# Kernel tuning notes

Hardware: AMD Instinct MI355X
Metric: run time of the kernel (lower is better)

## Reference

```python
import jax, jax.numpy as jnp
import numpy as np

INPUT_DIM = 16
HIDDEN_DIM = 2048
OUTPUT_DIM = 3
SEQ_LEN = 8192


def setup_inputs() -> dict:
    key = jax.random.key(0)
    ks = jax.random.split(key, 9)
    s = 1.0 / np.sqrt(HIDDEN_DIM)  # PyTorch LSTMCell/Linear init scale
    return {
        "state_action": jax.random.normal(ks[0], (SEQ_LEN, INPUT_DIM), dtype=jnp.float32),
        "W_ih": jax.random.uniform(ks[1], (4 * HIDDEN_DIM, INPUT_DIM), jnp.float32, -s, s),
        "W_hh": jax.random.uniform(ks[2], (4 * HIDDEN_DIM, HIDDEN_DIM), jnp.float32, -s, s),
        "b_ih": jax.random.uniform(ks[3], (4 * HIDDEN_DIM,), jnp.float32, -s, s),
        "b_hh": jax.random.uniform(ks[4], (4 * HIDDEN_DIM,), jnp.float32, -s, s),
        "W_uvw": jax.random.uniform(ks[5], (OUTPUT_DIM, HIDDEN_DIM), jnp.float32, -s, s),
        "b_uvw": jax.random.uniform(ks[6], (OUTPUT_DIM,), jnp.float32, -s, s),
        "W_pqr": jax.random.uniform(ks[7], (OUTPUT_DIM, HIDDEN_DIM), jnp.float32, -s, s),
        "b_pqr": jax.random.uniform(ks[8], (OUTPUT_DIM,), jnp.float32, -s, s),
    }


def reference(state_action, W_ih, W_hh, b_ih, b_hh, W_uvw, b_uvw, W_pqr, b_pqr):
    hd = W_hh.shape[1]
    # Precompute input projections for all timesteps: [H, 4*hd]
    x_proj = state_action @ W_ih.T + b_ih + b_hh

    def step(carry, xp):
        h, c = carry  # each [hd]
        gates = xp + h @ W_hh.T  # [4*hd]
        i, f, g, o = jnp.split(gates, 4)  # PyTorch gate order: input, forget, cell, output
        i = jax.nn.sigmoid(i)
        f = jax.nn.sigmoid(f)
        g = jnp.tanh(g)
        o = jax.nn.sigmoid(o)
        c_new = f * c + i * g
        h_new = o * jnp.tanh(c_new)
        return (h_new, c_new), h_new

    init = (jnp.zeros((hd,), jnp.float32), jnp.zeros((hd,), jnp.float32))
    _, hs = jax.lax.scan(step, init, x_proj)  # hs: [H, hd]

    uvw = hs @ W_uvw.T + b_uvw  # [H, 3]
    pqr = hs @ W_pqr.T + b_pqr  # [H, 3]
    # Original returns a list of [1, 6]; stacked+squeezed form is [H, 6]
    return jnp.concatenate([uvw, pqr], axis=-1)
```

## Files before the change

### kernel.cpp

```cpp
#include <hip/hip_runtime.h>
#include <cstdint>
#include <cstddef>

#define SEQ   8192
#define HD    2048
#define IND   16
#define NBLK  256
#define NTHR  256
#define NSLOT 1024
#define NXCD  8

#define GATE_TICKS 14ull

typedef _Float16 h2  __attribute__((ext_vector_type(2)));
typedef unsigned u32x4 __attribute__((ext_vector_type(4)));

union paircvt { h2 v; unsigned u; };

__device__ __forceinline__ float fdot2f(h2 a, h2 b, float c) {
#if defined(__has_builtin)
#if __has_builtin(__builtin_amdgcn_fdot2)
    return __builtin_amdgcn_fdot2(a, b, c, false);
#else
    return c + (float)a.x * (float)b.x + (float)a.y * (float)b.y;
#endif
#else
    return c + (float)a.x * (float)b.x + (float)a.y * (float)b.y;
#endif
}

__device__ __forceinline__ float sigmoid_f(float x) {
    return 1.f / (1.f + __expf(-x));
}
__device__ __forceinline__ float tanh_f(float x) {
    float e = __expf(2.f * x);
    return 1.f - 2.f / (e + 1.f);
}

__device__ __forceinline__ unsigned my_xcd() {
    unsigned x;
    asm volatile("s_getreg_b32 %0, hwreg(HW_REG_XCC_ID, 0, 4)" : "=s"(x));
    return x & (NXCD - 1);
}

__global__ __launch_bounds__(NTHR, 1) void lstm_persist(
    const float* __restrict__ sa,
    const float* __restrict__ W_ih,
    const float* __restrict__ W_hh,
    const float* __restrict__ b_ih,
    const float* __restrict__ b_hh,
    unsigned long long* __restrict__ hrep,
    _Float16* __restrict__ hs16)
{
    const int b   = blockIdx.x;
    const int tid = threadIdx.x;
    const int w   = tid >> 6;
    const int L   = tid & 63;
    const unsigned xcd = my_xcd();

    __shared__ h2 hh2[16 * 64];

    const int ubase = b * 8 + 2 * w;

    h2 wreg[8][16];
#pragma unroll
    for (int r = 0; r < 8; ++r) {
        const int row = (r & 3) * HD + ubase + (r >> 2);
        const float4* Wr = (const float4*)(W_hh + (size_t)row * HD + L * 32);
#pragma unroll
        for (int q = 0; q < 8; ++q) {
            float4 f = Wr[q];
            h2 lo; lo.x = (_Float16)f.x; lo.y = (_Float16)f.y;
            h2 hi; hi.x = (_Float16)f.z; hi.y = (_Float16)f.w;
            wreg[r][2 * q]     = lo;
            wreg[r][2 * q + 1] = hi;
        }
    }
    const int rowL = (L & 3) * HD + ubase + ((L >> 2) & 1);
    float wih[IND];
    {
        const float4* Wi = (const float4*)(W_ih + (size_t)rowL * IND);
#pragma unroll
        for (int q = 0; q < 4; ++q) {
            float4 f = Wi[q];
            wih[4 * q]     = f.x;
            wih[4 * q + 1] = f.y;
            wih[4 * q + 2] = f.z;
            wih[4 * q + 3] = f.w;
        }
    }
    const float bias = b_ih[rowL] + b_hh[rowL];

    float sat[IND];
    {
        const float4* s4 = (const float4*)(sa);
#pragma unroll
        for (int q = 0; q < 4; ++q) {
            float4 f = s4[q];
            sat[4 * q]     = f.x;
            sat[4 * q + 1] = f.y;
            sat[4 * q + 2] = f.z;
            sat[4 * q + 3] = f.w;
        }
    }

    float c = 0.f;
    unsigned long long pubclk = 0;

    for (unsigned t = 0; t < SEQ; ++t) {
        float xp = bias;
#pragma unroll
        for (int k = 0; k < IND; ++k) xp += sat[k] * wih[k];

        if (t + 1 < SEQ) {
            const float4* s4 = (const float4*)(sa + (size_t)(t + 1) * IND);
#pragma unroll
            for (int q = 0; q < 4; ++q) {
                float4 f = s4[q];
                sat[4 * q]     = f.x;
                sat[4 * q + 1] = f.y;
                sat[4 * q + 2] = f.z;
                sat[4 * q + 3] = f.w;
            }
        }

        if (t) {
            unsigned long long now;
            do {
                now = __builtin_amdgcn_s_memrealtime();
            } while (now - pubclk < GATE_TICKS);
        }

        const unsigned pin = t & 1;
        const uint32_t* base =
            (const uint32_t*)(hrep + ((size_t)xcd * 2 + pin) * NSLOT);
        const uint32_t* pp0 = base + 4 * tid;
        const uint32_t* pp1 = base + 1024 + 4 * tid;
        u32x4 m0, m1;
        int tries = 0;
        for (;;) {
            asm volatile(
                "global_load_dwordx4 %0, %2, off sc1\n\t"
                "global_load_dwordx4 %1, %3, off sc1\n\t"
                "s_waitcnt vmcnt(0)"
                : "=v"(m0), "=v"(m1)
                : "v"(pp0), "v"(pp1) : "memory");
            bool ok = (m0.y == t) & (m0.w == t) & (m1.y == t) & (m1.w == t);
            if (ok) break;
            if (++tries > 2) __builtin_amdgcn_s_sleep(1);
        }

        {
            paircvt cv;
            const int pa = 2 * tid, pb = 2 * tid + 1;
            const int pc = 512 + 2 * tid, pd = 513 + 2 * tid;
            cv.u = m0.x;
            hh2[(pa & 15) * 64 + (((pa >> 4) ^ (2 * (pa & 15))) & 63)] = cv.v;
            cv.u = m0.z;
            hh2[(pb & 15) * 64 + (((pb >> 4) ^ (2 * (pb & 15))) & 63)] = cv.v;
            cv.u = m1.x;
            hh2[(pc & 15) * 64 + (((pc >> 4) ^ (2 * (pc & 15))) & 63)] = cv.v;
            cv.u = m1.z;
            hh2[(pd & 15) * 64 + (((pd >> 4) ^ (2 * (pd & 15))) & 63)] = cv.v;
        }
        __syncthreads();

        h2 hv[16];
#pragma unroll
        for (int k = 0; k < 16; ++k)
            hv[k] = hh2[k * 64 + ((L ^ (2 * k)) & 63)];

        float p[8] = {0.f, 0.f, 0.f, 0.f, 0.f, 0.f, 0.f, 0.f};
#pragma unroll
        for (int r = 0; r < 8; ++r)
#pragma unroll
            for (int k = 0; k < 16; ++k)
                p[r] = fdot2f(wreg[r][k], hv[k], p[r]);

        const bool h1 = (L & 1), h2b = (L & 2), h4 = (L & 4);
        float v0, v1, v2, v3;
        {
            float k0 = h1 ? p[1] : p[0], s0 = h1 ? p[0] : p[1];
            v0 = k0 + __shfl_xor(s0, 1, 64);
            float k1 = h1 ? p[3] : p[2], s1 = h1 ? p[2] : p[3];
            v1 = k1 + __shfl_xor(s1, 1, 64);
            float k2 = h1 ? p[5] : p[4], s2 = h1 ? p[4] : p[5];
            v2 = k2 + __shfl_xor(s2, 1, 64);
            float k3 = h1 ? p[7] : p[6], s3 = h1 ? p[6] : p[7];
            v3 = k3 + __shfl_xor(s3, 1, 64);
        }
        float w0, w1;
        {
            float k0 = h2b ? v1 : v0, s0 = h2b ? v0 : v1;
            w0 = k0 + __shfl_xor(s0, 2, 64);
            float k1 = h2b ? v3 : v2, s1 = h2b ? v2 : v3;
            w1 = k1 + __shfl_xor(s1, 2, 64);
        }
        float tot;
        {
            float k0 = h4 ? w1 : w0, s0 = h4 ? w0 : w1;
            tot = k0 + __shfl_xor(s0, 4, 64);
        }
        tot += __shfl_xor(tot, 8, 64);
        tot += __shfl_xor(tot, 16, 64);
        tot += __shfl_xor(tot, 32, 64);
        tot += xp;

        const int ub4 = L & 4;
        float gi = __shfl(tot, ub4 + 0, 8);
        float gf = __shfl(tot, ub4 + 1, 8);
        float gg = __shfl(tot, ub4 + 2, 8);
        float go = __shfl(tot, ub4 + 3, 8);
        float ii = sigmoid_f(gi);
        float ff = sigmoid_f(gf);
        float g  = tanh_f(gg);
        float oo = sigmoid_f(go);
        c = ff * c + ii * g;
        float h = oo * tanh_f(c);

        {
            float hA = __shfl(h, 0, 8);
            float hB = __shfl(h, 4, 8);
            paircvt pk;
            pk.v.x = (_Float16)hA;
            pk.v.y = (_Float16)hB;
            const unsigned pout = (t + 1) & 1;
            const size_t slot = (size_t)b * 4 + w;
            unsigned long long msg =
                ((unsigned long long)(t + 1) << 32) | (unsigned long long)pk.u;
            if (L < 8)
                __hip_atomic_store(
                    &hrep[((size_t)L * 2 + pout) * NSLOT + slot], msg,
                    __ATOMIC_RELAXED, __HIP_MEMORY_SCOPE_AGENT);
            if (L == 0)
                ((unsigned*)hs16)[(size_t)t * (HD / 2) + b * 4 + w] = pk.u;
        }
        pubclk = __builtin_amdgcn_s_memrealtime();
    }
}

__global__ __launch_bounds__(256) void out_proj_kernel(
    const _Float16* __restrict__ hs16,
    const float* __restrict__ W_uvw, const float* __restrict__ b_uvw,
    const float* __restrict__ W_pqr, const float* __restrict__ b_pqr,
    float* __restrict__ out)
{
    __shared__ float Ws[6 * HD];
    const int tid = threadIdx.x;
    for (int i = tid; i < 3 * HD; i += 256) Ws[i] = W_uvw[i];
    for (int i = tid; i < 3 * HD; i += 256) Ws[3 * HD + i] = W_pqr[i];
    __syncthreads();

    const int w = tid >> 6, L = tid & 63;
#pragma unroll
    for (int r = 0; r < 4; ++r) {
        const int t = blockIdx.x * 16 + w * 4 + r;
        const _Float16* hrow = hs16 + (size_t)t * HD;
        float acc[6] = {0.f, 0.f, 0.f, 0.f, 0.f, 0.f};
        for (int cidx = L; cidx < HD; cidx += 64) {
            float hval = (float)hrow[cidx];
#pragma unroll
            for (int j = 0; j < 6; ++j) acc[j] += hval * Ws[j * HD + cidx];
        }
#pragma unroll
        for (int j = 0; j < 6; ++j) {
#pragma unroll
            for (int d = 1; d < 64; d <<= 1)
                acc[j] += __shfl_xor(acc[j], d, 64);
        }
        if (L == 0) {
#pragma unroll
            for (int j = 0; j < 6; ++j)
                out[(size_t)t * 6 + j] =
                    acc[j] + (j < 3 ? b_uvw[j] : b_pqr[j - 3]);
        }
    }
}

extern "C" void kernel_launch(void* const* d_in, const int* in_sizes, int n_in,
                              void* d_out, int out_size, void* d_ws, size_t ws_size,
                              hipStream_t stream) {
    (void)in_sizes; (void)n_in; (void)out_size; (void)ws_size;

    const float* sa    = (const float*)d_in[0];
    const float* W_ih  = (const float*)d_in[1];
    const float* W_hh  = (const float*)d_in[2];
    const float* b_ih  = (const float*)d_in[3];
    const float* b_hh  = (const float*)d_in[4];
    const float* W_uvw = (const float*)d_in[5];
    const float* b_uvw = (const float*)d_in[6];
    const float* W_pqr = (const float*)d_in[7];
    const float* b_pqr = (const float*)d_in[8];
    float* out = (float*)d_out;

    char* ws = (char*)d_ws;
    _Float16* hs16 = (_Float16*)ws;
    unsigned long long* hrep =
        (unsigned long long*)(ws + (size_t)SEQ * HD * 2);

    hipMemsetAsync(hrep, 0, (size_t)NXCD * 2 * NSLOT * 8, stream);

    hipLaunchKernelGGL(lstm_persist, dim3(NBLK), dim3(NTHR), 0, stream,
                       sa, W_ih, W_hh, b_ih, b_hh, hrep, hs16);
    hipLaunchKernelGGL(out_proj_kernel, dim3(SEQ / 16), dim3(256), 0, stream,
                       hs16, W_uvw, b_uvw, W_pqr, b_pqr, out);
}
```

Before: 15.24 ms.

## Split LSTM work to one hidden unit per wave with compact 32-bit messages

Blocks now run 512 threads, so each wave owns a single hidden unit (4 gate rows) instead of two units (8 rows). This halves the weight registers and the dot-product work per wave on the per-step critical path. The cross-block h exchange becomes one 32-bit word per unit, holding a 16-bit step tag and the fp16 h value, so each thread polls with a single 16-byte load. The gate reduction becomes a plain 6-step butterfly over four accumulators, with the input projection folded into one lane's accumulator. In exchange there are more waves per CU contending for sync and LDS, more shuffles per wave, and a 16-bit tag that only just fits the sequence length.

After: 20.01 ms. 1.31x slower.

```diff
diff --git a/kernel.cpp b/kernel.cpp
--- a/kernel.cpp
+++ b/kernel.cpp
@@ -6,8 +6,8 @@
 #define HD    2048
 #define IND   16
 #define NBLK  256
-#define NTHR  256
-#define NSLOT 1024
+#define NTHR  512
+#define NUNIT 2048
 #define NXCD  8
 
 #define GATE_TICKS 14ull
@@ -16,6 +16,7 @@
 typedef unsigned u32x4 __attribute__((ext_vector_type(4)));
 
 union paircvt { h2 v; unsigned u; };
+union hcvt { _Float16 f; unsigned short u; };
 
 __device__ __forceinline__ float fdot2f(h2 a, h2 b, float c) {
 #if defined(__has_builtin)
@@ -49,7 +50,7 @@
     const float* __restrict__ W_hh,
     const float* __restrict__ b_ih,
     const float* __restrict__ b_hh,
-    unsigned long long* __restrict__ hrep,
+    unsigned* __restrict__ hrep,
     _Float16* __restrict__ hs16)
 {
     const int b   = blockIdx.x;
@@ -60,12 +61,12 @@
 
     __shared__ h2 hh2[16 * 64];
 
-    const int ubase = b * 8 + 2 * w;
-
-    h2 wreg[8][16];
-#pragma unroll
-    for (int r = 0; r < 8; ++r) {
-        const int row = (r & 3) * HD + ubase + (r >> 2);
+    const int unit = b * 8 + w;
+
+    h2 wreg[4][16];
+#pragma unroll
+    for (int r = 0; r < 4; ++r) {
+        const int row = r * HD + unit;
         const float4* Wr = (const float4*)(W_hh + (size_t)row * HD + L * 32);
 #pragma unroll
         for (int q = 0; q < 8; ++q) {
@@ -76,7 +77,7 @@
             wreg[r][2 * q + 1] = hi;
         }
     }
-    const int rowL = (L & 3) * HD + ubase + ((L >> 2) & 1);
+    const int rowL = (L & 3) * HD + unit;
     float wih[IND];
     {
         const float4* Wi = (const float4*)(W_ih + (size_t)rowL * IND);
@@ -132,20 +133,18 @@
         }
 
         const unsigned pin = t & 1;
-        const uint32_t* base =
-            (const uint32_t*)(hrep + ((size_t)xcd * 2 + pin) * NSLOT);
-        const uint32_t* pp0 = base + 4 * tid;
-        const uint32_t* pp1 = base + 1024 + 4 * tid;
-        u32x4 m0, m1;
+        const uint32_t* pp =
+            (const uint32_t*)hrep + ((size_t)xcd * 2 + pin) * NUNIT + 4 * tid;
+        u32x4 m;
         int tries = 0;
         for (;;) {
             asm volatile(
-                "global_load_dwordx4 %0, %2, off sc1\n\t"
-                "global_load_dwordx4 %1, %3, off sc1\n\t"
+                "global_load_dwordx4 %0, %1, off sc1\n\t"
                 "s_waitcnt vmcnt(0)"
-                : "=v"(m0), "=v"(m1)
-                : "v"(pp0), "v"(pp1) : "memory");
-            bool ok = (m0.y == t) & (m0.w == t) & (m1.y == t) & (m1.w == t);
+                : "=v"(m)
+                : "v"(pp) : "memory");
+            bool ok = ((m.x >> 16) == t) & ((m.y >> 16) == t) &
+                      ((m.z >> 16) == t) & ((m.w >> 16) == t);
             if (ok) break;
             if (++tries > 2) __builtin_amdgcn_s_sleep(1);
         }
@@ -153,15 +152,10 @@
         {
             paircvt cv;
             const int pa = 2 * tid, pb = 2 * tid + 1;
-            const int pc = 512 + 2 * tid, pd = 513 + 2 * tid;
-            cv.u = m0.x;
+            cv.u = (m.y << 16) | (m.x & 0xffffu);
             hh2[(pa & 15) * 64 + (((pa >> 4) ^ (2 * (pa & 15))) & 63)] = cv.v;
-            cv.u = m0.z;
+            cv.u = (m.w << 16) | (m.z & 0xffffu);
             hh2[(pb & 15) * 64 + (((pb >> 4) ^ (2 * (pb & 15))) & 63)] = cv.v;
-            cv.u = m1.x;
-            hh2[(pc & 15) * 64 + (((pc >> 4) ^ (2 * (pc & 15))) & 63)] = cv.v;
-            cv.u = m1.z;
-            hh2[(pd & 15) * 64 + (((pd >> 4) ^ (2 * (pd & 15))) & 63)] = cv.v;
         }
         __syncthreads();
 
@@ -170,70 +164,43 @@
         for (int k = 0; k < 16; ++k)
             hv[k] = hh2[k * 64 + ((L ^ (2 * k)) & 63)];
 
-        float p[8] = {0.f, 0.f, 0.f, 0.f, 0.f, 0.f, 0.f, 0.f};
-#pragma unroll
-        for (int r = 0; r < 8; ++r)
-#pragma unroll
-            for (int k = 0; k < 16; ++k)
-                p[r] = fdot2f(wreg[r][k], hv[k], p[r]);
-
-        const bool h1 = (L & 1), h2b = (L & 2), h4 = (L & 4);
-        float v0, v1, v2, v3;
-        {
-            float k0 = h1 ? p[1] : p[0], s0 = h1 ? p[0] : p[1];
-            v0 = k0 + __shfl_xor(s0, 1, 64);
-            float k1 = h1 ? p[3] : p[2], s1 = h1 ? p[2] : p[3];
-            v1 = k1 + __shfl_xor(s1, 1, 64);
-            float k2 = h1 ? p[5] : p[4], s2 = h1 ? p[4] : p[5];
-            v2 = k2 + __shfl_xor(s2, 1, 64);
-            float k3 = h1 ? p[7] : p[6], s3 = h1 ? p[6] : p[7];
-            v3 = k3 + __shfl_xor(s3, 1, 64);
-        }
-        float w0, w1;
-        {
-            float k0 = h2b ? v1 : v0, s0 = h2b ? v0 : v1;
-            w0 = k0 + __shfl_xor(s0, 2, 64);
-            float k1 = h2b ? v3 : v2, s1 = h2b ? v2 : v3;
-            w1 = k1 + __shfl_xor(s1, 2, 64);
-        }
-        float tot;
-        {
-            float k0 = h4 ? w1 : w0, s0 = h4 ? w0 : w1;
-            tot = k0 + __shfl_xor(s0, 4, 64);
-        }
-        tot += __shfl_xor(tot, 8, 64);
-        tot += __shfl_xor(tot, 16, 64);
-        tot += __shfl_xor(tot, 32, 64);
-        tot += xp;
-
-        const int ub4 = L & 4;
-        float gi = __shfl(tot, ub4 + 0, 8);
-        float gf = __shfl(tot, ub4 + 1, 8);
-        float gg = __shfl(tot, ub4 + 2, 8);
-        float go = __shfl(tot, ub4 + 3, 8);
-        float ii = sigmoid_f(gi);
-        float ff = sigmoid_f(gf);
-        float g  = tanh_f(gg);
-        float oo = sigmoid_f(go);
+        float p0 = (L == 0) ? xp : 0.f;
+        float p1 = (L == 1) ? xp : 0.f;
+        float p2 = (L == 2) ? xp : 0.f;
+        float p3 = (L == 3) ? xp : 0.f;
+#pragma unroll
+        for (int k = 0; k < 16; ++k) {
+            p0 = fdot2f(wreg[0][k], hv[k], p0);
+            p1 = fdot2f(wreg[1][k], hv[k], p1);
+            p2 = fdot2f(wreg[2][k], hv[k], p2);
+            p3 = fdot2f(wreg[3][k], hv[k], p3);
+        }
+
+#pragma unroll
+        for (int d = 1; d < 64; d <<= 1) {
+            p0 += __shfl_xor(p0, d, 64);
+            p1 += __shfl_xor(p1, d, 64);
+            p2 += __shfl_xor(p2, d, 64);
+            p3 += __shfl_xor(p3, d, 64);
+        }
+
+        float ii = sigmoid_f(p0);
+        float ff = sigmoid_f(p1);
+        float g  = tanh_f(p2);
+        float oo = sigmoid_f(p3);
         c = ff * c + ii * g;
         float h = oo * tanh_f(c);
 
         {
-            float hA = __shfl(h, 0, 8);
-            float hB = __shfl(h, 4, 8);
-            paircvt pk;
-            pk.v.x = (_Float16)hA;
-            pk.v.y = (_Float16)hB;
+            hcvt hc; hc.f = (_Float16)h;
+            const unsigned msg = ((t + 1) << 16) | (unsigned)hc.u;
             const unsigned pout = (t + 1) & 1;
-            const size_t slot = (size_t)b * 4 + w;
-            unsigned long long msg =
-                ((unsigned long long)(t + 1) << 32) | (unsigned long long)pk.u;
             if (L < 8)
                 __hip_atomic_store(
-                    &hrep[((size_t)L * 2 + pout) * NSLOT + slot], msg,
+                    &hrep[((size_t)L * 2 + pout) * NUNIT + unit], msg,
                     __ATOMIC_RELAXED, __HIP_MEMORY_SCOPE_AGENT);
-            if (L == 0)
-                ((unsigned*)hs16)[(size_t)t * (HD / 2) + b * 4 + w] = pk.u;
+            if (L == 8)
+                hs16[(size_t)t * HD + unit] = (_Float16)h;
         }
         pubclk = __builtin_amdgcn_s_memrealtime();
     }
@@ -295,10 +262,9 @@
 
     char* ws = (char*)d_ws;
     _Float16* hs16 = (_Float16*)ws;
-    unsigned long long* hrep =
-        (unsigned long long*)(ws + (size_t)SEQ * HD * 2);
-
-    hipMemsetAsync(hrep, 0, (size_t)NXCD * 2 * NSLOT * 8, stream);
+    unsigned* hrep = (unsigned*)(ws + (size_t)SEQ * HD * 2);
+
+    hipMemsetAsync(hrep, 0, (size_t)NXCD * 2 * NUNIT * 4, stream);
 
     hipLaunchKernelGGL(lstm_persist, dim3(NBLK), dim3(NTHR), 0, stream,
                        sa, W_ih, W_hh, b_ih, b_hh, hrep, hs16);
```
